# Performance work log

Hardware: AMD Instinct MI355X
Metric: run time of the kernel (lower is better)

The kernel has to match this reference:

```python
import jax, jax.numpy as jnp
import numpy as np
from jax import lax

W_SIZE = 11
SIGMA = 1.5

def _gaussian_window(w_size, sigma, channel):
    x = np.arange(w_size) - w_size // 2
    g = np.exp(-(x.astype(np.float64) ** 2) / (2.0 * sigma ** 2))
    g = g / g.sum()
    w2d = np.outer(g, g).astype(np.float32)  # [w, w]
    # depthwise kernel in OIHW with feature_group_count=channel: [C, 1, w, w]
    return jnp.asarray(np.broadcast_to(w2d, (channel, 1, w_size, w_size)))

def _dwconv(x, window, channel):
    return lax.conv_general_dilated(
        x, window, window_strides=(1, 1), padding='VALID',
        dimension_numbers=('NCHW', 'OIHW', 'NCHW'),
        feature_group_count=channel)

def setup_inputs() -> dict:
    key = jax.random.key(0)
    k1, k2 = jax.random.split(key)
    B, C, H, W = 16, 3, 512, 512
    y_pred = jax.random.uniform(k1, (B, C, H, W), dtype=jnp.float32)
    y_true = jax.random.uniform(k2, (B, C, H, W), dtype=jnp.float32)
    return {"y_pred": y_pred, "y_true": y_true}

def reference(y_pred, y_true):
    channel = y_pred.shape[1]
    L = jnp.max(y_pred) - jnp.min(y_pred)
    window = _gaussian_window(W_SIZE, SIGMA, channel)

    mu1 = _dwconv(y_pred, window, channel)
    mu2 = _dwconv(y_true, window, channel)
    mu1_sq = mu1 * mu1
    mu2_sq = mu2 * mu2
    mu1_mu2 = mu1 * mu2
    sigma1_sq = _dwconv(y_pred * y_pred, window, channel) - mu1_sq
    sigma2_sq = _dwconv(y_true * y_true, window, channel) - mu2_sq
    sigma12 = _dwconv(y_pred * y_true, window, channel) - mu1_mu2

    C1 = (0.01 * L) ** 2
    C2 = (0.03 * L) ** 2
    v1 = 2.0 * sigma12 + C2
    v2 = sigma1_sq + sigma2_sq + C2
    ssim_map = (2.0 * mu1_mu2 + C1) * v1 / ((mu1_sq + mu2_sq + C1) * v2)
    # size_average=True, full=False defaults
    return -jnp.mean(ssim_map)
```

## Files before the change

kernel.cpp:

```cpp
#include <hip/hip_runtime.h>
#include <math.h>

#define WSZ   11
#define HALO  10
#define TW    32
#define TH    32
#define IN_W  (TW + HALO)
#define IN_H  (TH + HALO)
#define IMG_H 512
#define IMG_W 512
#define OUT_H (IMG_H - HALO)
#define OUT_W (IMG_W - HALO)
#define NBC   48


__device__ __forceinline__ unsigned enc_key(float f) {
    unsigned u = __float_as_uint(f);
    return (u & 0x80000000u) ? ~u : (u | 0x80000000u);
}
__device__ __forceinline__ float dec_key(unsigned k) {
    unsigned u = (k & 0x80000000u) ? (k ^ 0x80000000u) : ~k;
    return __uint_as_float(u);
}

__global__ void init_ws(unsigned* wsi, double* wsum) {
    wsi[0] = 0xFFFFFFFFu;
    wsi[1] = 0u;
    wsum[0] = 0.0;
}

__global__ __launch_bounds__(256) void minmax_kernel(const float4* __restrict__ x,
                                                     int n4, unsigned* wsi) {
    float lmin = INFINITY, lmax = -INFINITY;
    for (int i = blockIdx.x * blockDim.x + threadIdx.x; i < n4;
         i += gridDim.x * blockDim.x) {
        float4 v = x[i];
        lmin = fminf(lmin, fminf(fminf(v.x, v.y), fminf(v.z, v.w)));
        lmax = fmaxf(lmax, fmaxf(fmaxf(v.x, v.y), fmaxf(v.z, v.w)));
    }
    for (int o = 32; o; o >>= 1) {
        lmin = fminf(lmin, __shfl_xor(lmin, o));
        lmax = fmaxf(lmax, __shfl_xor(lmax, o));
    }
    __shared__ float smin[4], smax[4];
    int tid = threadIdx.x;
    if ((tid & 63) == 0) { smin[tid >> 6] = lmin; smax[tid >> 6] = lmax; }
    __syncthreads();
    if (tid == 0) {
        float m0 = fminf(fminf(smin[0], smin[1]), fminf(smin[2], smin[3]));
        float m1 = fmaxf(fmaxf(smax[0], smax[1]), fmaxf(smax[2], smax[3]));
        atomicMin(&wsi[0], enc_key(m0));
        atomicMax(&wsi[1], enc_key(m1));
    }
}

__global__ __launch_bounds__(256) void ssim_kernel(const float* __restrict__ x,
                                                   const float* __restrict__ y,
                                                   const unsigned* __restrict__ wsi,
                                                   double* wsum) {
    __shared__ float sx[IN_H][IN_W];
    __shared__ float sy[IN_H][IN_W];
    __shared__ float hbuf[5][IN_H][TW];
    __shared__ float gwin[WSZ];
    __shared__ float wpart[4];

    const int tid = threadIdx.x;
    if (tid == 0) {
        double g[WSZ], s = 0.0;
        #pragma unroll
        for (int i = 0; i < WSZ; i++) {
            double d = (double)(i - WSZ / 2);
            g[i] = exp(-(d * d) / (2.0 * 1.5 * 1.5));
            s += g[i];
        }
        #pragma unroll
        for (int i = 0; i < WSZ; i++) gwin[i] = (float)(g[i] / s);
    }

    const int bc  = blockIdx.x;
    const int oy0 = blockIdx.y * TH;
    const int ox0 = blockIdx.z * TW;
    const float* xb = x + (size_t)bc * IMG_H * IMG_W;
    const float* yb = y + (size_t)bc * IMG_H * IMG_W;

    for (int idx = tid; idx < IN_H * IN_W; idx += 256) {
        int r = idx / IN_W, c = idx % IN_W;
        int gy = min(oy0 + r, IMG_H - 1);
        int gx = min(ox0 + c, IMG_W - 1);
        float xv = xb[gy * IMG_W + gx];
        float yv = yb[gy * IMG_W + gx];
        sx[r][c] = xv;
        sy[r][c] = yv;
    }
    __syncthreads();

    for (int idx = tid; idx < IN_H * TW; idx += 256) {
        int r = idx >> 5, c = idx & 31;
        float a0 = 0.f, a1 = 0.f, a2 = 0.f, a3 = 0.f, a4 = 0.f;
        #pragma unroll
        for (int k = 0; k < WSZ; k++) {
            float w  = gwin[k];
            float xv = sx[r][c + k];
            float yv = sy[r][c + k];
            a0 += w * xv;
            a1 += w * yv;
            a2 += w * xv * xv;
            a3 += w * yv * yv;
            a4 += w * xv * yv;
        }
        hbuf[0][r][c] = a0;
        hbuf[1][r][c] = a1;
        hbuf[2][r][c] = a2;
        hbuf[3][r][c] = a3;
        hbuf[4][r][c] = a4;
    }
    __syncthreads();

    float fmin_v = dec_key(wsi[0]);
    float fmax_v = dec_key(wsi[1]);
    float L  = fmax_v - fmin_v;
    float C1 = 0.01f * L; C1 *= C1;
    float C2 = 0.03f * L; C2 *= C2;

    float lsum = 0.f;
    for (int idx = tid; idx < TH * TW; idx += 256) {
        int r = idx >> 5, c = idx & 31;
        int oy = oy0 + r, ox = ox0 + c;
        if (oy < OUT_H && ox < OUT_W) {
            float m1 = 0.f, m2 = 0.f, e11 = 0.f, e22 = 0.f, e12 = 0.f;
            #pragma unroll
            for (int k = 0; k < WSZ; k++) {
                float w = gwin[k];
                m1  += w * hbuf[0][r + k][c];
                m2  += w * hbuf[1][r + k][c];
                e11 += w * hbuf[2][r + k][c];
                e22 += w * hbuf[3][r + k][c];
                e12 += w * hbuf[4][r + k][c];
            }
            float mu1s = m1 * m1, mu2s = m2 * m2, m12 = m1 * m2;
            float s1  = e11 - mu1s;
            float s2  = e22 - mu2s;
            float s12 = e12 - m12;
            float v1  = 2.f * s12 + C2;
            float v2  = s1 + s2 + C2;
            float num = (2.f * m12 + C1) * v1;
            float den = (mu1s + mu2s + C1) * v2;
            lsum += num / den;
        }
    }

    for (int o = 32; o; o >>= 1) lsum += __shfl_xor(lsum, o);
    if ((tid & 63) == 0) wpart[tid >> 6] = lsum;
    __syncthreads();
    if (tid == 0) {
        double t = (double)wpart[0] + (double)wpart[1] +
                   (double)wpart[2] + (double)wpart[3];
        atomicAdd(wsum, t);
    }
}

__global__ void finalize_kernel(const double* wsum, float* out) {
    const double count = (double)NBC * OUT_H * OUT_W;
    out[0] = (float)(-wsum[0] / count);
}

extern "C" void kernel_launch(void* const* d_in, const int* in_sizes, int n_in,
                              void* d_out, int out_size, void* d_ws, size_t ws_size,
                              hipStream_t stream) {
    (void)n_in; (void)out_size; (void)ws_size;
    const float* y_pred = (const float*)d_in[0];
    const float* y_true = (const float*)d_in[1];
    float* out = (float*)d_out;

    unsigned* wsi = (unsigned*)d_ws;
    double* wsum = (double*)((char*)d_ws + 8);

    init_ws<<<1, 1, 0, stream>>>(wsi, wsum);

    int n4 = in_sizes[0] / 4;
    minmax_kernel<<<2048, 256, 0, stream>>>((const float4*)y_pred, n4, wsi);

    dim3 grid(NBC, (OUT_H + TH - 1) / TH, (OUT_W + TW - 1) / TW);
    ssim_kernel<<<grid, 256, 0, stream>>>(y_pred, y_true, wsi, wsum);

    finalize_kernel<<<1, 1, 0, stream>>>(wsum, out);
}
```

Before: 311.4 us.

## Register-block separable SSIM conv with float4 loads and taller tiles

Tiles grow to 64x32 outputs and the image loads become float4. Each thread now computes 4 columns in the horizontal pass and a 4x2 output block in the vertical pass, keeping the inputs in registers so the shared-memory reads are reused across outputs. The Gaussian weights are computed on the host and passed as kernel arguments, and the division becomes a reciprocal plus one Newton step. This cuts LDS traffic and halo overhead, at the cost of more registers per thread and an approximate reciprocal.

```diff
diff --git a/kernel.cpp b/kernel.cpp
--- a/kernel.cpp
+++ b/kernel.cpp
@@ -1,17 +1,16 @@
 #include <hip/hip_runtime.h>
 #include <math.h>
 
-#define WSZ   11
-#define HALO  10
+#define IMG   512
+#define OUTD  502
+#define NBC   48
+#define TH    64
 #define TW    32
-#define TH    32
-#define IN_W  (TW + HALO)
-#define IN_H  (TH + HALO)
-#define IMG_H 512
-#define IMG_W 512
-#define OUT_H (IMG_H - HALO)
-#define OUT_W (IMG_W - HALO)
-#define NBC   48
+#define IN_ROWS (TH + 10)
+#define SXW   44
+#define HBW   32
+
+struct WParams { float w[11]; };
 
 
 __device__ __forceinline__ unsigned enc_key(float f) {
@@ -57,64 +56,74 @@
 __global__ __launch_bounds__(256) void ssim_kernel(const float* __restrict__ x,
                                                    const float* __restrict__ y,
                                                    const unsigned* __restrict__ wsi,
-                                                   double* wsum) {
-    __shared__ float sx[IN_H][IN_W];
-    __shared__ float sy[IN_H][IN_W];
-    __shared__ float hbuf[5][IN_H][TW];
-    __shared__ float gwin[WSZ];
+                                                   double* __restrict__ wsum,
+                                                   WParams P) {
+    __shared__ __align__(16) float sx[IN_ROWS * SXW];
+    __shared__ __align__(16) float sy[IN_ROWS * SXW];
+    __shared__ __align__(16) float hb[5 * IN_ROWS * HBW];
     __shared__ float wpart[4];
 
     const int tid = threadIdx.x;
-    if (tid == 0) {
-        double g[WSZ], s = 0.0;
-        #pragma unroll
-        for (int i = 0; i < WSZ; i++) {
-            double d = (double)(i - WSZ / 2);
-            g[i] = exp(-(d * d) / (2.0 * 1.5 * 1.5));
-            s += g[i];
-        }
-        #pragma unroll
-        for (int i = 0; i < WSZ; i++) gwin[i] = (float)(g[i] / s);
-    }
-
     const int bc  = blockIdx.x;
     const int oy0 = blockIdx.y * TH;
     const int ox0 = blockIdx.z * TW;
-    const float* xb = x + (size_t)bc * IMG_H * IMG_W;
-    const float* yb = y + (size_t)bc * IMG_H * IMG_W;
-
-    for (int idx = tid; idx < IN_H * IN_W; idx += 256) {
-        int r = idx / IN_W, c = idx % IN_W;
-        int gy = min(oy0 + r, IMG_H - 1);
-        int gx = min(ox0 + c, IMG_W - 1);
-        float xv = xb[gy * IMG_W + gx];
-        float yv = yb[gy * IMG_W + gx];
-        sx[r][c] = xv;
-        sy[r][c] = yv;
-    }
-    __syncthreads();
-
-    for (int idx = tid; idx < IN_H * TW; idx += 256) {
-        int r = idx >> 5, c = idx & 31;
-        float a0 = 0.f, a1 = 0.f, a2 = 0.f, a3 = 0.f, a4 = 0.f;
-        #pragma unroll
-        for (int k = 0; k < WSZ; k++) {
-            float w  = gwin[k];
-            float xv = sx[r][c + k];
-            float yv = sy[r][c + k];
-            a0 += w * xv;
-            a1 += w * yv;
-            a2 += w * xv * xv;
-            a3 += w * yv * yv;
-            a4 += w * xv * yv;
-        }
-        hbuf[0][r][c] = a0;
-        hbuf[1][r][c] = a1;
-        hbuf[2][r][c] = a2;
-        hbuf[3][r][c] = a3;
-        hbuf[4][r][c] = a4;
-    }
-    __syncthreads();
+    const float* xb = x + (size_t)bc * IMG * IMG;
+    const float* yb = y + (size_t)bc * IMG * IMG;
+
+    for (int idx = tid; idx < IN_ROWS * 11; idx += 256) {
+        int r = idx / 11, g = idx - r * 11;
+        int gy = min(oy0 + r, IMG - 1);
+        int gx = min(ox0 + 4 * g, IMG - 4);
+        float4 vx = *(const float4*)(xb + gy * IMG + gx);
+        float4 vy = *(const float4*)(yb + gy * IMG + gx);
+        *(float4*)(sx + r * SXW + 4 * g) = vx;
+        *(float4*)(sy + r * SXW + 4 * g) = vy;
+    }
+    __syncthreads();
+
+    for (int idx = tid; idx < IN_ROWS * 8; idx += 256) {
+        int r = idx >> 3, g = idx & 7;
+        int c = 4 * g;
+        const float* rx = sx + r * SXW + c;
+        const float* ry = sy + r * SXW + c;
+        float xr[16], yr[16];
+        #pragma unroll
+        for (int q = 0; q < 4; q++) {
+            float4 a = *(const float4*)(rx + 4 * q);
+            float4 b = *(const float4*)(ry + 4 * q);
+            xr[4*q] = a.x; xr[4*q+1] = a.y; xr[4*q+2] = a.z; xr[4*q+3] = a.w;
+            yr[4*q] = b.x; yr[4*q+1] = b.y; yr[4*q+2] = b.z; yr[4*q+3] = b.w;
+        }
+        float xx[14], yy[14], xy[14];
+        #pragma unroll
+        for (int e = 0; e < 14; e++) {
+            xx[e] = xr[e] * xr[e];
+            yy[e] = yr[e] * yr[e];
+            xy[e] = xr[e] * yr[e];
+        }
+        float acc[5][4];
+        #pragma unroll
+        for (int ch = 0; ch < 5; ch++)
+            #pragma unroll
+            for (int j = 0; j < 4; j++) acc[ch][j] = 0.f;
+        #pragma unroll
+        for (int k = 0; k < 11; k++) {
+            float w = P.w[k];
+            #pragma unroll
+            for (int j = 0; j < 4; j++) {
+                acc[0][j] += w * xr[j + k];
+                acc[1][j] += w * yr[j + k];
+                acc[2][j] += w * xx[j + k];
+                acc[3][j] += w * yy[j + k];
+                acc[4][j] += w * xy[j + k];
+            }
+        }
+        #pragma unroll
+        for (int ch = 0; ch < 5; ch++) {
+            float4 v = make_float4(acc[ch][0], acc[ch][1], acc[ch][2], acc[ch][3]);
+            *(float4*)(hb + (ch * IN_ROWS + r) * HBW + c) = v;
+        }
+    }
 
     float fmin_v = dec_key(wsi[0]);
     float fmax_v = dec_key(wsi[1]);
@@ -122,30 +131,57 @@
     float C1 = 0.01f * L; C1 *= C1;
     float C2 = 0.03f * L; C2 *= C2;
 
+    __syncthreads();
+
+    const int q  = tid & 15;
+    const int rr = tid >> 4;
+    const int r0 = 4 * rr;
+    const int c  = 2 * q;
+
+    float2 acc[5][4];
+    #pragma unroll
+    for (int ch = 0; ch < 5; ch++)
+        #pragma unroll
+        for (int o = 0; o < 4; o++) { acc[ch][o].x = 0.f; acc[ch][o].y = 0.f; }
+
+    #pragma unroll
+    for (int k = 0; k < 14; k++) {
+        #pragma unroll
+        for (int ch = 0; ch < 5; ch++) {
+            float2 v = *(const float2*)(hb + (ch * IN_ROWS + r0 + k) * HBW + c);
+            #pragma unroll
+            for (int o = 0; o < 4; o++) {
+                int t = k - o;
+                if (t >= 0 && t <= 10) {
+                    acc[ch][o].x += P.w[t] * v.x;
+                    acc[ch][o].y += P.w[t] * v.y;
+                }
+            }
+        }
+    }
+
     float lsum = 0.f;
-    for (int idx = tid; idx < TH * TW; idx += 256) {
-        int r = idx >> 5, c = idx & 31;
-        int oy = oy0 + r, ox = ox0 + c;
-        if (oy < OUT_H && ox < OUT_W) {
-            float m1 = 0.f, m2 = 0.f, e11 = 0.f, e22 = 0.f, e12 = 0.f;
-            #pragma unroll
-            for (int k = 0; k < WSZ; k++) {
-                float w = gwin[k];
-                m1  += w * hbuf[0][r + k][c];
-                m2  += w * hbuf[1][r + k][c];
-                e11 += w * hbuf[2][r + k][c];
-                e22 += w * hbuf[3][r + k][c];
-                e12 += w * hbuf[4][r + k][c];
+    #pragma unroll
+    for (int o = 0; o < 4; o++) {
+        int oy = oy0 + r0 + o;
+        #pragma unroll
+        for (int cc = 0; cc < 2; cc++) {
+            int ox = ox0 + c + cc;
+            if (oy < OUTD && ox < OUTD) {
+                float m1  = cc ? acc[0][o].y : acc[0][o].x;
+                float m2  = cc ? acc[1][o].y : acc[1][o].x;
+                float e11 = cc ? acc[2][o].y : acc[2][o].x;
+                float e22 = cc ? acc[3][o].y : acc[3][o].x;
+                float e12 = cc ? acc[4][o].y : acc[4][o].x;
+                float m1s = m1 * m1, m2s = m2 * m2, m12 = m1 * m2;
+                float v1  = 2.f * (e12 - m12) + C2;
+                float v2  = (e11 - m1s) + (e22 - m2s) + C2;
+                float num = (2.f * m12 + C1) * v1;
+                float den = (m1s + m2s + C1) * v2;
+                float rc  = __builtin_amdgcn_rcpf(den);
+                rc = rc * (2.f - den * rc);
+                lsum += num * rc;
             }
-            float mu1s = m1 * m1, mu2s = m2 * m2, m12 = m1 * m2;
-            float s1  = e11 - mu1s;
-            float s2  = e22 - mu2s;
-            float s12 = e12 - m12;
-            float v1  = 2.f * s12 + C2;
-            float v2  = s1 + s2 + C2;
-            float num = (2.f * m12 + C1) * v1;
-            float den = (mu1s + mu2s + C1) * v2;
-            lsum += num / den;
         }
     }
 
@@ -160,7 +196,7 @@
 }
 
 __global__ void finalize_kernel(const double* wsum, float* out) {
-    const double count = (double)NBC * OUT_H * OUT_W;
+    const double count = (double)NBC * OUTD * OUTD;
     out[0] = (float)(-wsum[0] / count);
 }
 
@@ -175,13 +211,24 @@
     unsigned* wsi = (unsigned*)d_ws;
     double* wsum = (double*)((char*)d_ws + 8);
 
+    WParams P;
+    {
+        double g[11], s = 0.0;
+        for (int i = 0; i < 11; i++) {
+            double d = (double)(i - 5);
+            g[i] = exp(-(d * d) / (2.0 * 1.5 * 1.5));
+            s += g[i];
+        }
+        for (int i = 0; i < 11; i++) P.w[i] = (float)(g[i] / s);
+    }
+
     init_ws<<<1, 1, 0, stream>>>(wsi, wsum);
 
     int n4 = in_sizes[0] / 4;
     minmax_kernel<<<2048, 256, 0, stream>>>((const float4*)y_pred, n4, wsi);
 
-    dim3 grid(NBC, (OUT_H + TH - 1) / TH, (OUT_W + TW - 1) / TW);
-    ssim_kernel<<<grid, 256, 0, stream>>>(y_pred, y_true, wsi, wsum);
+    dim3 grid(NBC, (OUTD + TH - 1) / TH, (OUTD + TW - 1) / TW);
+    ssim_kernel<<<grid, 256, 0, stream>>>(y_pred, y_true, wsi, wsum, P);
 
     finalize_kernel<<<1, 1, 0, stream>>>(wsum, out);
 }
```

After: 249.4 us. 19.9% less time.
